# Kernel tuning notes

Measured on AMD Instinct MI355X. Metric: run time of the kernel, lower is better.

Reference implementation:

```python
import jax, jax.numpy as jnp
import numpy as np

B, C, D = 64, 1000, 2048
SCALE_CONF = 10.0   # confidence scale in forward
SCALE_COS = 16.0    # CosNorm_Classifier default scale


def setup_inputs() -> dict:
    key = jax.random.key(0)
    ks = jax.random.split(key, 8)
    x = jax.random.normal(ks[0], (B, D), jnp.float32)
    labels = jax.random.randint(ks[1], (B,), 0, C)
    centers = jax.random.normal(ks[2], (C, D), jnp.float32)
    class_count = jax.random.randint(ks[3], (C,), 0, 100)
    # learned parameters
    fc_channel_w = jax.random.normal(ks[4], (D, D), jnp.float32) * 0.02
    fc_channel_b = jnp.zeros((D,), jnp.float32)
    fc1_w = jax.random.normal(ks[5], (C, D), jnp.float32) * 0.02
    fc1_b = jnp.zeros((C,), jnp.float32)
    cos_w = jax.random.normal(ks[6], (C, D), jnp.float32) * 0.001
    return {"x": x, "labels": labels, "centers": centers, "class_count": class_count,
            "fc_channel_w": fc_channel_w, "fc_channel_b": fc_channel_b,
            "fc1_w": fc1_w, "fc1_b": fc1_b, "cos_w": cos_w}


def reference(x, labels, centers, class_count, fc_channel_w, fc_channel_b, fc1_w, fc1_b, cos_w):
    # pairwise L2 distance to all class centers; only the per-row min is used
    # downstream, so we fuse the sort-then-take-first into a min reduction.
    x2 = jnp.sum(x * x, axis=1, keepdims=True)            # [B,1]
    c2 = jnp.sum(centers * centers, axis=1)               # [C]
    d2 = jnp.maximum(x2 - 2.0 * (x @ centers.T) + c2[None, :], 0.0)  # [B,C]
    min_dist = jnp.sqrt(jnp.min(d2, axis=1, keepdims=True))          # [B,1] == values_nn[:,0]
    confidence = SCALE_CONF / min_dist                    # broadcasts over feat dim

    # stage-1 classifier -> soft assignment to centers (memory hallucination)
    logits_stage1 = x @ fc1_w.T + fc1_b                   # [B,C]
    prob_stage1 = jax.nn.softmax(logits_stage1, axis=1)
    centers_cur = prob_stage1 @ centers                   # [B,D]

    channel_selector = jnp.tanh(x @ fc_channel_w.T + fc_channel_b)  # [B,D]
    slow_feature = x
    fast_feature = channel_selector * centers_cur
    x_new = confidence * (x + fast_feature)               # [B,D]

    # CosNorm_Classifier: ex = (|x|/(1+|x|)) * x/|x|; ew = w/|w|; logits = scale*ex @ ew.T
    norm_x = jnp.linalg.norm(x_new, axis=1, keepdims=True)
    ex = (norm_x / (1.0 + norm_x)) * (x_new / norm_x)
    ew = cos_w / jnp.linalg.norm(cos_w, axis=1, keepdims=True)
    logits = (SCALE_COS * ex) @ ew.T                      # [B,C]

    return logits, slow_feature, fast_feature
```

## Files before the change

### kernel.cpp

```cpp
#include <hip/hip_runtime.h>
#include <hip/hip_bf16.h>
#include <math.h>

typedef __attribute__((ext_vector_type(8))) short short8;
typedef __attribute__((ext_vector_type(4))) float f32x4;

#define MFMA(a, b, c) __builtin_amdgcn_mfma_f32_16x16x32_bf16(a, b, c, 0, 0, 0)

enum : int {
  WS_XB    = 0,
  WS_X2    = 65536,
  WS_DMINP = 65600,
  WS_SPART = 69696,
  WS_PROB  = 73792,
  WS_SEL   = 106560,
  WS_XNB   = 172096,
  WS_XN2P  = 237632,
  WS_CTB   = 245824,
};

__device__ inline short bfs(float f) {
  __hip_bfloat16 h = __float2bfloat16(f);
  return __builtin_bit_cast(short, h);
}
__device__ inline float bf2f(unsigned short u) {
  return __uint_as_float((unsigned)u << 16);
}

__device__ inline void gload16(const float* g, float* lds) {
  __builtin_amdgcn_global_load_lds(
      (const __attribute__((address_space(1))) unsigned int*)g,
      (__attribute__((address_space(3))) unsigned int*)lds, 16, 0, 0);
}

__global__ __launch_bounds__(256) void k1(const float* __restrict__ x,
                                          const float* __restrict__ centers,
                                          float* __restrict__ out,
                                          float* __restrict__ ws) {
  __shared__ float A[64][65];
  int blk = blockIdx.x, t = threadIdx.x;
  int l = t & 63, w = t >> 6;
  if (blk < 64) {
    int b = blk;
    const float* xr = x + (size_t)b * 2048 + t * 8;
    float4 f0 = *(const float4*)(xr);
    float4 f1 = *(const float4*)(xr + 4);
    short8 h;
    h[0] = bfs(f0.x); h[1] = bfs(f0.y); h[2] = bfs(f0.z); h[3] = bfs(f0.w);
    h[4] = bfs(f1.x); h[5] = bfs(f1.y); h[6] = bfs(f1.z); h[7] = bfs(f1.w);
    *(short8*)((unsigned short*)(ws + WS_XB) + (size_t)b * 2048 + t * 8) = h;
    *(float4*)(out + 64000 + (size_t)b * 2048 + t * 8) = f0;
    *(float4*)(out + 64000 + (size_t)b * 2048 + t * 8 + 4) = f1;
    float s = f0.x*f0.x + f0.y*f0.y + f0.z*f0.z + f0.w*f0.w
            + f1.x*f1.x + f1.y*f1.y + f1.z*f1.z + f1.w*f1.w;
#pragma unroll
    for (int o = 32; o; o >>= 1) s += __shfl_xor(s, o);
    if (l == 0) A[0][w] = s;
    __syncthreads();
    if (t == 0) ws[WS_X2 + b] = A[0][0] + A[0][1] + A[0][2] + A[0][3];
  } else {
    int tid = blk - 64;
    int tc = tid & 15, td = tid >> 4;
    int c0 = tc * 64, d0 = td * 64;
    for (int r = 0; r < 16; ++r) {
      int cc = r * 4 + w;
      int c = c0 + cc;
      A[cc][l] = (c < 1000) ? centers[(size_t)c * 2048 + d0 + l] : 0.f;
    }
    __syncthreads();
    unsigned short* ctb = (unsigned short*)(ws + WS_CTB);
    for (int r = 0; r < 16; ++r) {
      int dd = r * 4 + w;
      ctb[(size_t)(d0 + dd) * 1024 + c0 + l] = (unsigned short)bfs(A[l][dd]);
    }
  }
}

__global__ __launch_bounds__(512) void k2(const float* __restrict__ centers,
                                          const float* __restrict__ fc1w,
                                          const float* __restrict__ fcw,
                                          const float* __restrict__ fc1b,
                                          const float* __restrict__ fcb,
                                          float* __restrict__ ws) {
  __shared__ float WT[2][16][1028];
  __shared__ f32x4 sacc[8][64];
  __shared__ float ssq[8][64];
  int blk = blockIdx.x, t = threadIdx.x;
  int w = t >> 6, l = t & 63;
  int ln = l & 15, lk = l >> 4;
  int n0 = blk * 16;
  bool cen = (n0 < 1024);

  auto stage = [&](int buf, int koff) {
    for (int r = 0; r < 2; ++r) {
      int row = w * 2 + r;
      int n = n0 + row;
      const float* brow;
      if (n < 1024)      brow = centers + (size_t)min(n, 999) * 2048;
      else if (n < 2048) brow = fc1w + (size_t)min(n - 1024, 999) * 2048;
      else               brow = fcw + (size_t)(n - 2048) * 2048;
#pragma unroll
      for (int j = 0; j < 4; ++j)
        gload16(brow + koff + j * 256 + l * 4, &WT[buf][row][j * 256]);
    }
  };

  stage(0, 0);
  __syncthreads();
  stage(1, 1024);

  int m0 = (w & 3) * 16;
  int kq = (w >> 2) * 512;
  const unsigned short* aptr =
      (const unsigned short*)(ws + WS_XB) + (size_t)(m0 + ln) * 2048 + kq + lk * 8;
  f32x4 acc = {0.f, 0.f, 0.f, 0.f};
  float sq = 0.f;

  {
    const float* wrow = &WT[0][ln][kq + lk * 8];
#pragma unroll 4
    for (int ks = 0; ks < 16; ++ks) {
      short8 a0 = *(const short8*)(aptr + ks * 32);
      float4 f0 = *(const float4*)(wrow + ks * 32);
      float4 f1 = *(const float4*)(wrow + ks * 32 + 4);
      if (cen)
        sq += f0.x*f0.x + f0.y*f0.y + f0.z*f0.z + f0.w*f0.w
            + f1.x*f1.x + f1.y*f1.y + f1.z*f1.z + f1.w*f1.w;
      short8 bb;
      bb[0] = bfs(f0.x); bb[1] = bfs(f0.y); bb[2] = bfs(f0.z); bb[3] = bfs(f0.w);
      bb[4] = bfs(f1.x); bb[5] = bfs(f1.y); bb[6] = bfs(f1.z); bb[7] = bfs(f1.w);
      acc = MFMA(a0, bb, acc);
    }
  }
  __syncthreads();
  {
    const float* wrow = &WT[1][ln][kq + lk * 8];
    const unsigned short* ap1 = aptr + 1024;
#pragma unroll 4
    for (int ks = 0; ks < 16; ++ks) {
      short8 a0 = *(const short8*)(ap1 + ks * 32);
      float4 f0 = *(const float4*)(wrow + ks * 32);
      float4 f1 = *(const float4*)(wrow + ks * 32 + 4);
      if (cen)
        sq += f0.x*f0.x + f0.y*f0.y + f0.z*f0.z + f0.w*f0.w
            + f1.x*f1.x + f1.y*f1.y + f1.z*f1.z + f1.w*f1.w;
      short8 bb;
      bb[0] = bfs(f0.x); bb[1] = bfs(f0.y); bb[2] = bfs(f0.z); bb[3] = bfs(f0.w);
      bb[4] = bfs(f1.x); bb[5] = bfs(f1.y); bb[6] = bfs(f1.z); bb[7] = bfs(f1.w);
      acc = MFMA(a0, bb, acc);
    }
  }

  sacc[w][l] = acc;
  ssq[w][l] = sq;
  __syncthreads();
  if (w < 4) {
    f32x4 a2 = sacc[w + 4][l];
    acc.x += a2.x; acc.y += a2.y; acc.z += a2.z; acc.w += a2.w;
    sq = ssq[w][l] + ssq[w + 4][l];

    if (cen) {
      sq += __shfl_xor(sq, 16);
      sq += __shfl_xor(sq, 32);
      int colv = n0 + ln;
#pragma unroll
      for (int j = 0; j < 4; ++j) {
        int m = m0 + lk * 4 + j;
        float d2 = (colv < 1000)
            ? fmaxf(ws[WS_X2 + m] - 2.f * acc[j] + sq, 0.f) : 3.0e38f;
        d2 = fminf(d2, __shfl_xor(d2, 1));
        d2 = fminf(d2, __shfl_xor(d2, 2));
        d2 = fminf(d2, __shfl_xor(d2, 4));
        d2 = fminf(d2, __shfl_xor(d2, 8));
        if (ln == 0) ws[WS_DMINP + blk * 64 + m] = d2;
      }
    } else if (n0 < 2048) {
      int c = n0 - 1024 + ln;
      unsigned short* pb = (unsigned short*)(ws + WS_PROB);
#pragma unroll
      for (int j = 0; j < 4; ++j) {
        int m = m0 + lk * 4 + j;
        float e = (c < 1000) ? __expf(acc[j] + fc1b[c]) : 0.f;
        pb[(size_t)m * 1024 + c] = (unsigned short)bfs(e);
        float s = e;
        s += __shfl_xor(s, 1);
        s += __shfl_xor(s, 2);
        s += __shfl_xor(s, 4);
        s += __shfl_xor(s, 8);
        if (ln == 0) ws[WS_SPART + (blk - 64) * 64 + m] = s;
      }
    } else {
      int d = n0 - 2048 + ln;
      unsigned short* sel = (unsigned short*)(ws + WS_SEL);
#pragma unroll
      for (int j = 0; j < 4; ++j) {
        int m = m0 + lk * 4 + j;
        float sv = tanhf(acc[j] + fcb[d]);
        sel[(size_t)m * 2048 + d] = (unsigned short)bfs(sv);
      }
    }
  }
}

__global__ __launch_bounds__(256) void kde(const float* __restrict__ x,
                                           float* __restrict__ out,
                                           float* __restrict__ ws) {
  __shared__ f32x4 sacc[4][2][64];
  __shared__ float sinv[64];
  int blk = blockIdx.x, t = threadIdx.x;
  int w = t >> 6, l = t & 63;
  int cs = blk >> 1, mh = blk & 1;
  int d0 = cs * 16, m0 = mh * 32;
  int ln = l & 15, lk = l >> 4;
  int k0 = w * 256;
  if (t < 64) {
    float s = 0.f;
#pragma unroll
    for (int i = 0; i < 64; ++i) s += ws[WS_SPART + i * 64 + t];
    sinv[t] = 1.0f / s;
  }
  const unsigned short* aptr =
      (const unsigned short*)(ws + WS_PROB) + (size_t)(m0 + ln) * 1024 + k0 + lk * 8;
  const unsigned short* brow =
      (const unsigned short*)(ws + WS_CTB) + (size_t)(d0 + ln) * 1024 + k0 + lk * 8;
  f32x4 acc0 = {0.f, 0.f, 0.f, 0.f}, acc1 = {0.f, 0.f, 0.f, 0.f};
#pragma unroll
  for (int ks = 0; ks < 8; ++ks) {
    short8 a0 = *(const short8*)(aptr + ks * 32);
    short8 a1 = *(const short8*)(aptr + 16 * 1024 + ks * 32);
    short8 bb = *(const short8*)(brow + ks * 32);
    acc0 = MFMA(a0, bb, acc0);
    acc1 = MFMA(a1, bb, acc1);
  }
  sacc[w][0][l] = acc0;
  sacc[w][1][l] = acc1;
  __syncthreads();
  if (w == 0) {
    f32x4 r0 = sacc[0][0][l], r1 = sacc[0][1][l];
#pragma unroll
    for (int i = 1; i < 4; ++i) {
      f32x4 u0 = sacc[i][0][l], u1 = sacc[i][1][l];
      r0.x += u0.x; r0.y += u0.y; r0.z += u0.z; r0.w += u0.w;
      r1.x += u1.x; r1.y += u1.y; r1.z += u1.z; r1.w += u1.w;
    }
    const unsigned short* sel = (const unsigned short*)(ws + WS_SEL);
    unsigned short* xnb = (unsigned short*)(ws + WS_XNB);
    float rr[8] = {r0.x, r0.y, r0.z, r0.w, r1.x, r1.y, r1.z, r1.w};
#pragma unroll
    for (int q = 0; q < 8; ++q) {
      int b = m0 + (q >> 2) * 16 + lk * 4 + (q & 3);
      int d = d0 + ln;
      float cc = rr[q] * sinv[b];
      float sv = bf2f(sel[(size_t)b * 2048 + d]);
      float xv = x[(size_t)b * 2048 + d];
      float fast = sv * cc;
      out[195072 + (size_t)b * 2048 + d] = fast;
      float yv = xv + fast;
      xnb[(size_t)b * 2048 + d] = (unsigned short)bfs(yv);
      float sq = yv * yv;
      sq += __shfl_xor(sq, 1);
      sq += __shfl_xor(sq, 2);
      sq += __shfl_xor(sq, 4);
      sq += __shfl_xor(sq, 8);
      if (ln == 0) ws[WS_XN2P + cs * 64 + b] = sq;
    }
  }
}

__global__ __launch_bounds__(512) void k7(const float* __restrict__ cosw,
                                          float* __restrict__ out,
                                          float* __restrict__ ws) {
  __shared__ float WT[2][16][1028];
  __shared__ f32x4 sacc[8][64];
  __shared__ float ssq[8][64];
  __shared__ float scale_s[64];
  int blk = blockIdx.x, t = threadIdx.x;
  int w = t >> 6, l = t & 63;
  int ln = l & 15, lk = l >> 4;
  int n0 = blk * 16;

  if (t < 64) {
    float s = 0.f;
    for (int i = 0; i < 128; ++i) s += ws[WS_XN2P + i * 64 + t];
    float ny = sqrtf(fmaxf(s, 0.f));
    float d2 = 3.0e38f;
    for (int i = 0; i < 64; ++i) d2 = fminf(d2, ws[WS_DMINP + i * 64 + t]);
    float cf = 10.0f * rsqrtf(fmaxf(d2, 1e-20f));
    scale_s[t] = 16.0f * cf / (1.0f + cf * ny);
  }

  auto stage = [&](int buf, int koff) {
    for (int r = 0; r < 2; ++r) {
      int row = w * 2 + r;
      const float* brow = cosw + (size_t)min(n0 + row, 999) * 2048;
#pragma unroll
      for (int j = 0; j < 4; ++j)
        gload16(brow + koff + j * 256 + l * 4, &WT[buf][row][j * 256]);
    }
  };

  stage(0, 0);
  __syncthreads();
  stage(1, 1024);

  int m0 = (w & 3) * 16;
  int kq = (w >> 2) * 512;
  const unsigned short* aptr =
      (const unsigned short*)(ws + WS_XNB) + (size_t)(m0 + ln) * 2048 + kq + lk * 8;
  f32x4 acc = {0.f, 0.f, 0.f, 0.f};
  float sq = 0.f;

  {
    const float* wrow = &WT[0][ln][kq + lk * 8];
#pragma unroll 4
    for (int ks = 0; ks < 16; ++ks) {
      short8 a0 = *(const short8*)(aptr + ks * 32);
      float4 f0 = *(const float4*)(wrow + ks * 32);
      float4 f1 = *(const float4*)(wrow + ks * 32 + 4);
      sq += f0.x*f0.x + f0.y*f0.y + f0.z*f0.z + f0.w*f0.w
          + f1.x*f1.x + f1.y*f1.y + f1.z*f1.z + f1.w*f1.w;
      short8 bb;
      bb[0] = bfs(f0.x); bb[1] = bfs(f0.y); bb[2] = bfs(f0.z); bb[3] = bfs(f0.w);
      bb[4] = bfs(f1.x); bb[5] = bfs(f1.y); bb[6] = bfs(f1.z); bb[7] = bfs(f1.w);
      acc = MFMA(a0, bb, acc);
    }
  }
  __syncthreads();
  {
    const float* wrow = &WT[1][ln][kq + lk * 8];
    const unsigned short* ap1 = aptr + 1024;
#pragma unroll 4
    for (int ks = 0; ks < 16; ++ks) {
      short8 a0 = *(const short8*)(ap1 + ks * 32);
      float4 f0 = *(const float4*)(wrow + ks * 32);
      float4 f1 = *(const float4*)(wrow + ks * 32 + 4);
      sq += f0.x*f0.x + f0.y*f0.y + f0.z*f0.z + f0.w*f0.w
          + f1.x*f1.x + f1.y*f1.y + f1.z*f1.z + f1.w*f1.w;
      short8 bb;
      bb[0] = bfs(f0.x); bb[1] = bfs(f0.y); bb[2] = bfs(f0.z); bb[3] = bfs(f0.w);
      bb[4] = bfs(f1.x); bb[5] = bfs(f1.y); bb[6] = bfs(f1.z); bb[7] = bfs(f1.w);
      acc = MFMA(a0, bb, acc);
    }
  }

  sacc[w][l] = acc;
  ssq[w][l] = sq;
  __syncthreads();
  if (w < 4) {
    f32x4 a2 = sacc[w + 4][l];
    acc.x += a2.x; acc.y += a2.y; acc.z += a2.z; acc.w += a2.w;
    sq = ssq[w][l] + ssq[w + 4][l];
    sq += __shfl_xor(sq, 16);
    sq += __shfl_xor(sq, 32);
    float invw = rsqrtf(fmaxf(sq, 1e-30f));
    int c = n0 + ln;
    if (c < 1000) {
#pragma unroll
      for (int j = 0; j < 4; ++j) {
        int m = m0 + lk * 4 + j;
        out[(size_t)m * 1000 + c] = acc[j] * invw * scale_s[m];
      }
    }
  }
}

extern "C" void kernel_launch(void* const* d_in, const int* in_sizes, int n_in,
                              void* d_out, int out_size, void* d_ws, size_t ws_size,
                              hipStream_t stream) {
  const float* x       = (const float*)d_in[0];
  const float* centers = (const float*)d_in[2];
  const float* fcw     = (const float*)d_in[4];
  const float* fcb     = (const float*)d_in[5];
  const float* fc1w    = (const float*)d_in[6];
  const float* fc1b    = (const float*)d_in[7];
  const float* cosw    = (const float*)d_in[8];
  float* out = (float*)d_out;
  float* ws  = (float*)d_ws;

  hipLaunchKernelGGL(k1,  dim3(576), dim3(256), 0, stream, x, centers, out, ws);
  hipLaunchKernelGGL(k2,  dim3(256), dim3(512), 0, stream, centers, fc1w, fcw, fc1b, fcb, ws);
  hipLaunchKernelGGL(kde, dim3(256), dim3(256), 0, stream, x, out, ws);
  hipLaunchKernelGGL(k7,  dim3(64),  dim3(512), 0, stream, cosw, out, ws);
}
```

Measured before the change: 58.65 us.

## Fuse prep kernel into GEMM kernel and defer x2 term to final stage

Removes the separate k1 launch by folding the x copy/x-norm and centers transpose-to-bf16 work into extra blocks of k2. The GEMM blocks now read x in fp32 directly and convert it to bf16 in registers, so the bf16 staging buffer for x is gone. Because the x² term no longer exists when the GEMM finishes, the per-row min is taken over (c² - 2x·c) and x² is added back in k7. This saves one launch and the dependency between kernels, at the cost of doubled global reads of x and extra conversion work inside the GEMM loop.

```diff
diff --git a/kernel.cpp b/kernel.cpp
--- a/kernel.cpp
+++ b/kernel.cpp
@@ -8,7 +8,6 @@
 #define MFMA(a, b, c) __builtin_amdgcn_mfma_f32_16x16x32_bf16(a, b, c, 0, 0, 0)
 
 enum : int {
-  WS_XB    = 0,
   WS_X2    = 65536,
   WS_DMINP = 65600,
   WS_SPART = 69696,
@@ -33,54 +32,13 @@
       (__attribute__((address_space(3))) unsigned int*)lds, 16, 0, 0);
 }
 
-__global__ __launch_bounds__(256) void k1(const float* __restrict__ x,
+__global__ __launch_bounds__(512) void k2(const float* __restrict__ x,
                                           const float* __restrict__ centers,
-                                          float* __restrict__ out,
-                                          float* __restrict__ ws) {
-  __shared__ float A[64][65];
-  int blk = blockIdx.x, t = threadIdx.x;
-  int l = t & 63, w = t >> 6;
-  if (blk < 64) {
-    int b = blk;
-    const float* xr = x + (size_t)b * 2048 + t * 8;
-    float4 f0 = *(const float4*)(xr);
-    float4 f1 = *(const float4*)(xr + 4);
-    short8 h;
-    h[0] = bfs(f0.x); h[1] = bfs(f0.y); h[2] = bfs(f0.z); h[3] = bfs(f0.w);
-    h[4] = bfs(f1.x); h[5] = bfs(f1.y); h[6] = bfs(f1.z); h[7] = bfs(f1.w);
-    *(short8*)((unsigned short*)(ws + WS_XB) + (size_t)b * 2048 + t * 8) = h;
-    *(float4*)(out + 64000 + (size_t)b * 2048 + t * 8) = f0;
-    *(float4*)(out + 64000 + (size_t)b * 2048 + t * 8 + 4) = f1;
-    float s = f0.x*f0.x + f0.y*f0.y + f0.z*f0.z + f0.w*f0.w
-            + f1.x*f1.x + f1.y*f1.y + f1.z*f1.z + f1.w*f1.w;
-#pragma unroll
-    for (int o = 32; o; o >>= 1) s += __shfl_xor(s, o);
-    if (l == 0) A[0][w] = s;
-    __syncthreads();
-    if (t == 0) ws[WS_X2 + b] = A[0][0] + A[0][1] + A[0][2] + A[0][3];
-  } else {
-    int tid = blk - 64;
-    int tc = tid & 15, td = tid >> 4;
-    int c0 = tc * 64, d0 = td * 64;
-    for (int r = 0; r < 16; ++r) {
-      int cc = r * 4 + w;
-      int c = c0 + cc;
-      A[cc][l] = (c < 1000) ? centers[(size_t)c * 2048 + d0 + l] : 0.f;
-    }
-    __syncthreads();
-    unsigned short* ctb = (unsigned short*)(ws + WS_CTB);
-    for (int r = 0; r < 16; ++r) {
-      int dd = r * 4 + w;
-      ctb[(size_t)(d0 + dd) * 1024 + c0 + l] = (unsigned short)bfs(A[l][dd]);
-    }
-  }
-}
-
-__global__ __launch_bounds__(512) void k2(const float* __restrict__ centers,
                                           const float* __restrict__ fc1w,
                                           const float* __restrict__ fcw,
                                           const float* __restrict__ fc1b,
                                           const float* __restrict__ fcb,
+                                          float* __restrict__ out,
                                           float* __restrict__ ws) {
   __shared__ float WT[2][16][1028];
   __shared__ f32x4 sacc[8][64];
@@ -88,6 +46,44 @@
   int blk = blockIdx.x, t = threadIdx.x;
   int w = t >> 6, l = t & 63;
   int ln = l & 15, lk = l >> 4;
+
+  if (blk >= 256 && blk < 320) {
+    int b = blk - 256;
+    float4 f = *(const float4*)(x + (size_t)b * 2048 + t * 4);
+    *(float4*)(out + 64000 + (size_t)b * 2048 + t * 4) = f;
+    float s = f.x * f.x + f.y * f.y + f.z * f.z + f.w * f.w;
+#pragma unroll
+    for (int o = 32; o; o >>= 1) s += __shfl_xor(s, o);
+    float* red8 = &ssq[0][0];
+    if (l == 0) red8[w] = s;
+    __syncthreads();
+    if (t == 0) {
+      float tot = 0.f;
+#pragma unroll
+      for (int i = 0; i < 8; ++i) tot += red8[i];
+      ws[WS_X2 + b] = tot;
+    }
+    return;
+  }
+  if (blk >= 320) {
+    float(*A)[65] = (float(*)[65]) & WT[0][0][0];
+    int tid = blk - 320;
+    int tc = tid & 15, td = tid >> 4;
+    int c0 = tc * 64, d0 = td * 64;
+    for (int r = 0; r < 8; ++r) {
+      int cc = r * 8 + w;
+      int c = c0 + cc;
+      A[cc][l] = (c < 1000) ? centers[(size_t)c * 2048 + d0 + l] : 0.f;
+    }
+    __syncthreads();
+    unsigned short* ctb = (unsigned short*)(ws + WS_CTB);
+    for (int r = 0; r < 8; ++r) {
+      int dd = r * 8 + w;
+      ctb[(size_t)(d0 + dd) * 1024 + c0 + l] = (unsigned short)bfs(A[l][dd]);
+    }
+    return;
+  }
+
   int n0 = blk * 16;
   bool cen = (n0 < 1024);
 
@@ -111,40 +107,27 @@
 
   int m0 = (w & 3) * 16;
   int kq = (w >> 2) * 512;
-  const unsigned short* aptr =
-      (const unsigned short*)(ws + WS_XB) + (size_t)(m0 + ln) * 2048 + kq + lk * 8;
+  const float* xrow = x + (size_t)(m0 + ln) * 2048 + kq + lk * 8;
   f32x4 acc = {0.f, 0.f, 0.f, 0.f};
   float sq = 0.f;
 
-  {
-    const float* wrow = &WT[0][ln][kq + lk * 8];
+#pragma unroll 2
+  for (int ch = 0; ch < 2; ++ch) {
+    if (ch == 1) __syncthreads();
+    const float* wrow = &WT[ch][ln][kq + lk * 8];
+    const float* xp = xrow + ch * 1024;
 #pragma unroll 4
     for (int ks = 0; ks < 16; ++ks) {
-      short8 a0 = *(const short8*)(aptr + ks * 32);
+      float4 g0 = *(const float4*)(xp + ks * 32);
+      float4 g1 = *(const float4*)(xp + ks * 32 + 4);
       float4 f0 = *(const float4*)(wrow + ks * 32);
       float4 f1 = *(const float4*)(wrow + ks * 32 + 4);
       if (cen)
         sq += f0.x*f0.x + f0.y*f0.y + f0.z*f0.z + f0.w*f0.w
             + f1.x*f1.x + f1.y*f1.y + f1.z*f1.z + f1.w*f1.w;
-      short8 bb;
-      bb[0] = bfs(f0.x); bb[1] = bfs(f0.y); bb[2] = bfs(f0.z); bb[3] = bfs(f0.w);
-      bb[4] = bfs(f1.x); bb[5] = bfs(f1.y); bb[6] = bfs(f1.z); bb[7] = bfs(f1.w);
-      acc = MFMA(a0, bb, acc);
-    }
-  }
-  __syncthreads();
-  {
-    const float* wrow = &WT[1][ln][kq + lk * 8];
-    const unsigned short* ap1 = aptr + 1024;
-#pragma unroll 4
-    for (int ks = 0; ks < 16; ++ks) {
-      short8 a0 = *(const short8*)(ap1 + ks * 32);
-      float4 f0 = *(const float4*)(wrow + ks * 32);
-      float4 f1 = *(const float4*)(wrow + ks * 32 + 4);
-      if (cen)
-        sq += f0.x*f0.x + f0.y*f0.y + f0.z*f0.z + f0.w*f0.w
-            + f1.x*f1.x + f1.y*f1.y + f1.z*f1.z + f1.w*f1.w;
-      short8 bb;
+      short8 a0, bb;
+      a0[0] = bfs(g0.x); a0[1] = bfs(g0.y); a0[2] = bfs(g0.z); a0[3] = bfs(g0.w);
+      a0[4] = bfs(g1.x); a0[5] = bfs(g1.y); a0[6] = bfs(g1.z); a0[7] = bfs(g1.w);
       bb[0] = bfs(f0.x); bb[1] = bfs(f0.y); bb[2] = bfs(f0.z); bb[3] = bfs(f0.w);
       bb[4] = bfs(f1.x); bb[5] = bfs(f1.y); bb[6] = bfs(f1.z); bb[7] = bfs(f1.w);
       acc = MFMA(a0, bb, acc);
@@ -166,13 +149,12 @@
 #pragma unroll
       for (int j = 0; j < 4; ++j) {
         int m = m0 + lk * 4 + j;
-        float d2 = (colv < 1000)
-            ? fmaxf(ws[WS_X2 + m] - 2.f * acc[j] + sq, 0.f) : 3.0e38f;
-        d2 = fminf(d2, __shfl_xor(d2, 1));
-        d2 = fminf(d2, __shfl_xor(d2, 2));
-        d2 = fminf(d2, __shfl_xor(d2, 4));
-        d2 = fminf(d2, __shfl_xor(d2, 8));
-        if (ln == 0) ws[WS_DMINP + blk * 64 + m] = d2;
+        float v2 = (colv < 1000) ? (sq - 2.f * acc[j]) : 3.0e38f;
+        v2 = fminf(v2, __shfl_xor(v2, 1));
+        v2 = fminf(v2, __shfl_xor(v2, 2));
+        v2 = fminf(v2, __shfl_xor(v2, 4));
+        v2 = fminf(v2, __shfl_xor(v2, 8));
+        if (ln == 0) ws[WS_DMINP + blk * 64 + m] = v2;
       }
     } else if (n0 < 2048) {
       int c = n0 - 1024 + ln;
@@ -283,8 +265,9 @@
     float s = 0.f;
     for (int i = 0; i < 128; ++i) s += ws[WS_XN2P + i * 64 + t];
     float ny = sqrtf(fmaxf(s, 0.f));
-    float d2 = 3.0e38f;
-    for (int i = 0; i < 64; ++i) d2 = fminf(d2, ws[WS_DMINP + i * 64 + t]);
+    float dmin = 3.0e38f;
+    for (int i = 0; i < 64; ++i) dmin = fminf(dmin, ws[WS_DMINP + i * 64 + t]);
+    float d2 = fmaxf(ws[WS_X2 + t] + dmin, 0.f);
     float cf = 10.0f * rsqrtf(fmaxf(d2, 1e-20f));
     scale_s[t] = 16.0f * cf / (1.0f + cf * ny);
   }
@@ -310,28 +293,14 @@
   f32x4 acc = {0.f, 0.f, 0.f, 0.f};
   float sq = 0.f;
 
-  {
-    const float* wrow = &WT[0][ln][kq + lk * 8];
+#pragma unroll 2
+  for (int ch = 0; ch < 2; ++ch) {
+    if (ch == 1) __syncthreads();
+    const float* wrow = &WT[ch][ln][kq + lk * 8];
+    const unsigned short* ap = aptr + ch * 1024;
 #pragma unroll 4
     for (int ks = 0; ks < 16; ++ks) {
-      short8 a0 = *(const short8*)(aptr + ks * 32);
-      float4 f0 = *(const float4*)(wrow + ks * 32);
-      float4 f1 = *(const float4*)(wrow + ks * 32 + 4);
-      sq += f0.x*f0.x + f0.y*f0.y + f0.z*f0.z + f0.w*f0.w
-          + f1.x*f1.x + f1.y*f1.y + f1.z*f1.z + f1.w*f1.w;
-      short8 bb;
-      bb[0] = bfs(f0.x); bb[1] = bfs(f0.y); bb[2] = bfs(f0.z); bb[3] = bfs(f0.w);
-      bb[4] = bfs(f1.x); bb[5] = bfs(f1.y); bb[6] = bfs(f1.z); bb[7] = bfs(f1.w);
-      acc = MFMA(a0, bb, acc);
-    }
-  }
-  __syncthreads();
-  {
-    const float* wrow = &WT[1][ln][kq + lk * 8];
-    const unsigned short* ap1 = aptr + 1024;
-#pragma unroll 4
-    for (int ks = 0; ks < 16; ++ks) {
-      short8 a0 = *(const short8*)(ap1 + ks * 32);
+      short8 a0 = *(const short8*)(ap + ks * 32);
       float4 f0 = *(const float4*)(wrow + ks * 32);
       float4 f1 = *(const float4*)(wrow + ks * 32 + 4);
       sq += f0.x*f0.x + f0.y*f0.y + f0.z*f0.z + f0.w*f0.w
@@ -377,8 +346,8 @@
   float* out = (float*)d_out;
   float* ws  = (float*)d_ws;
 
-  hipLaunchKernelGGL(k1,  dim3(576), dim3(256), 0, stream, x, centers, out, ws);
-  hipLaunchKernelGGL(k2,  dim3(256), dim3(512), 0, stream, centers, fc1w, fcw, fc1b, fcb, ws);
+  hipLaunchKernelGGL(k2,  dim3(832), dim3(512), 0, stream,
+                     x, centers, fc1w, fcw, fc1b, fcb, out, ws);
   hipLaunchKernelGGL(kde, dim3(256), dim3(256), 0, stream, x, out, ws);
   hipLaunchKernelGGL(k7,  dim3(64),  dim3(512), 0, stream, cosw, out, ws);
 }
```

Result: slower. 63.00 us (+7.4%).

## Pipeline k2 over four K-chunks and prefetch cos_w into L2 during kde

Applied to the files above, without the earlier changes.

k2 now stages weights in four 512-wide chunks with a smaller LDS double buffer, preloading the A operand per chunk and issuing the next chunk's loads before computing the current one. It also adds launch-bounds occupancy hints. kde gets 64 extra blocks that read all of cos_w and discard the sums, to warm the cache before k7 runs. The warm-up blocks add memory traffic and compete for CUs with kde's real work, and the more frequent syncs in k2 may cost as much as the overlap gains.

```diff
diff --git a/kernel.cpp b/kernel.cpp
--- a/kernel.cpp
+++ b/kernel.cpp
@@ -76,13 +76,13 @@
   }
 }
 
-__global__ __launch_bounds__(512) void k2(const float* __restrict__ centers,
-                                          const float* __restrict__ fc1w,
-                                          const float* __restrict__ fcw,
-                                          const float* __restrict__ fc1b,
-                                          const float* __restrict__ fcb,
-                                          float* __restrict__ ws) {
-  __shared__ float WT[2][16][1028];
+__global__ __launch_bounds__(512, 4) void k2(const float* __restrict__ centers,
+                                             const float* __restrict__ fc1w,
+                                             const float* __restrict__ fcw,
+                                             const float* __restrict__ fc1b,
+                                             const float* __restrict__ fcb,
+                                             float* __restrict__ ws) {
+  __shared__ float WT[2][16][516];
   __shared__ f32x4 sacc[8][64];
   __shared__ float ssq[8][64];
   int blk = blockIdx.x, t = threadIdx.x;
@@ -100,27 +100,32 @@
       else if (n < 2048) brow = fc1w + (size_t)min(n - 1024, 999) * 2048;
       else               brow = fcw + (size_t)(n - 2048) * 2048;
 #pragma unroll
-      for (int j = 0; j < 4; ++j)
+      for (int j = 0; j < 2; ++j)
         gload16(brow + koff + j * 256 + l * 4, &WT[buf][row][j * 256]);
     }
   };
 
-  stage(0, 0);
-  __syncthreads();
-  stage(1, 1024);
-
   int m0 = (w & 3) * 16;
-  int kq = (w >> 2) * 512;
+  int kq = (w >> 2) * 256;
   const unsigned short* aptr =
       (const unsigned short*)(ws + WS_XB) + (size_t)(m0 + ln) * 2048 + kq + lk * 8;
+
+  stage(0, 0);
+  __syncthreads();
+
   f32x4 acc = {0.f, 0.f, 0.f, 0.f};
   float sq = 0.f;
 
-  {
-    const float* wrow = &WT[0][ln][kq + lk * 8];
-#pragma unroll 4
-    for (int ks = 0; ks < 16; ++ks) {
-      short8 a0 = *(const short8*)(aptr + ks * 32);
+#pragma unroll
+  for (int ch = 0; ch < 4; ++ch) {
+    short8 A0[8];
+    const unsigned short* ap = aptr + ch * 512;
+#pragma unroll
+    for (int ks = 0; ks < 8; ++ks) A0[ks] = *(const short8*)(ap + ks * 32);
+    if (ch < 3) stage((ch + 1) & 1, (ch + 1) * 512);
+    const float* wrow = &WT[ch & 1][ln][kq + lk * 8];
+#pragma unroll
+    for (int ks = 0; ks < 8; ++ks) {
       float4 f0 = *(const float4*)(wrow + ks * 32);
       float4 f1 = *(const float4*)(wrow + ks * 32 + 4);
       if (cen)
@@ -129,26 +134,9 @@
       short8 bb;
       bb[0] = bfs(f0.x); bb[1] = bfs(f0.y); bb[2] = bfs(f0.z); bb[3] = bfs(f0.w);
       bb[4] = bfs(f1.x); bb[5] = bfs(f1.y); bb[6] = bfs(f1.z); bb[7] = bfs(f1.w);
-      acc = MFMA(a0, bb, acc);
-    }
-  }
-  __syncthreads();
-  {
-    const float* wrow = &WT[1][ln][kq + lk * 8];
-    const unsigned short* ap1 = aptr + 1024;
-#pragma unroll 4
-    for (int ks = 0; ks < 16; ++ks) {
-      short8 a0 = *(const short8*)(ap1 + ks * 32);
-      float4 f0 = *(const float4*)(wrow + ks * 32);
-      float4 f1 = *(const float4*)(wrow + ks * 32 + 4);
-      if (cen)
-        sq += f0.x*f0.x + f0.y*f0.y + f0.z*f0.z + f0.w*f0.w
-            + f1.x*f1.x + f1.y*f1.y + f1.z*f1.z + f1.w*f1.w;
-      short8 bb;
-      bb[0] = bfs(f0.x); bb[1] = bfs(f0.y); bb[2] = bfs(f0.z); bb[3] = bfs(f0.w);
-      bb[4] = bfs(f1.x); bb[5] = bfs(f1.y); bb[6] = bfs(f1.z); bb[7] = bfs(f1.w);
-      acc = MFMA(a0, bb, acc);
-    }
+      acc = MFMA(A0[ks], bb, acc);
+    }
+    if (ch < 3) __syncthreads();
   }
 
   sacc[w][l] = acc;
@@ -203,12 +191,28 @@
 }
 
 __global__ __launch_bounds__(256) void kde(const float* __restrict__ x,
+                                           const float* __restrict__ cosw,
                                            float* __restrict__ out,
                                            float* __restrict__ ws) {
   __shared__ f32x4 sacc[4][2][64];
   __shared__ float sinv[64];
   int blk = blockIdx.x, t = threadIdx.x;
   int w = t >> 6, l = t & 63;
+  if (blk >= 256) {
+    int p = blk - 256;
+    const float4* src = (const float4*)cosw;
+    int base = p * 8192;
+    float4 a = {0.f, 0.f, 0.f, 0.f};
+    for (int i = t; i < 8192; i += 256) {
+      int idx = base + i;
+      if (idx < 512000) {
+        float4 v = src[idx];
+        a.x += v.x; a.y += v.y; a.z += v.z; a.w += v.w;
+      }
+    }
+    asm volatile("" :: "v"(a.x), "v"(a.y), "v"(a.z), "v"(a.w));
+    return;
+  }
   int cs = blk >> 1, mh = blk & 1;
   int d0 = cs * 16, m0 = mh * 32;
   int ln = l & 15, lk = l >> 4;
@@ -310,28 +314,14 @@
   f32x4 acc = {0.f, 0.f, 0.f, 0.f};
   float sq = 0.f;
 
-  {
-    const float* wrow = &WT[0][ln][kq + lk * 8];
+#pragma unroll 2
+  for (int ch = 0; ch < 2; ++ch) {
+    if (ch == 1) __syncthreads();
+    const float* wrow = &WT[ch][ln][kq + lk * 8];
+    const unsigned short* ap = aptr + ch * 1024;
 #pragma unroll 4
     for (int ks = 0; ks < 16; ++ks) {
-      short8 a0 = *(const short8*)(aptr + ks * 32);
-      float4 f0 = *(const float4*)(wrow + ks * 32);
-      float4 f1 = *(const float4*)(wrow + ks * 32 + 4);
-      sq += f0.x*f0.x + f0.y*f0.y + f0.z*f0.z + f0.w*f0.w
-          + f1.x*f1.x + f1.y*f1.y + f1.z*f1.z + f1.w*f1.w;
-      short8 bb;
-      bb[0] = bfs(f0.x); bb[1] = bfs(f0.y); bb[2] = bfs(f0.z); bb[3] = bfs(f0.w);
-      bb[4] = bfs(f1.x); bb[5] = bfs(f1.y); bb[6] = bfs(f1.z); bb[7] = bfs(f1.w);
-      acc = MFMA(a0, bb, acc);
-    }
-  }
-  __syncthreads();
-  {
-    const float* wrow = &WT[1][ln][kq + lk * 8];
-    const unsigned short* ap1 = aptr + 1024;
-#pragma unroll 4
-    for (int ks = 0; ks < 16; ++ks) {
-      short8 a0 = *(const short8*)(ap1 + ks * 32);
+      short8 a0 = *(const short8*)(ap + ks * 32);
       float4 f0 = *(const float4*)(wrow + ks * 32);
       float4 f1 = *(const float4*)(wrow + ks * 32 + 4);
       sq += f0.x*f0.x + f0.y*f0.y + f0.z*f0.z + f0.w*f0.w
@@ -379,6 +369,6 @@
 
   hipLaunchKernelGGL(k1,  dim3(576), dim3(256), 0, stream, x, centers, out, ws);
   hipLaunchKernelGGL(k2,  dim3(256), dim3(512), 0, stream, centers, fc1w, fcw, fc1b, fcb, ws);
-  hipLaunchKernelGGL(kde, dim3(256), dim3(256), 0, stream, x, out, ws);
+  hipLaunchKernelGGL(kde, dim3(320), dim3(256), 0, stream, x, cosw, out, ws);
   hipLaunchKernelGGL(k7,  dim3(64),  dim3(512), 0, stream, cosw, out, ws);
 }
```

Result: slower. 61.27 us (+4.5%).
